# Optimization experiments

Measured on AMD Instinct MI355X. Metric: run time of the kernel, lower is better.

## Reference

```python
import jax, jax.numpy as jnp
import numpy as np

IN_CH = 64
OUT_CH = 64
MODES = 16
BATCH, H, W = 16, 128, 128


def setup_inputs() -> dict:
    key = jax.random.key(0)
    k1, k2, k3 = jax.random.split(key, 3)
    scale = 1.0 / (IN_CH * OUT_CH)
    x = jax.random.normal(k1, (BATCH, H, W, IN_CH), dtype=jnp.float32)
    weights_real = (scale * jax.random.normal(k2, (IN_CH, OUT_CH, MODES, MODES))).astype(jnp.float32)
    weights_imag = (scale * jax.random.normal(k3, (IN_CH, OUT_CH, MODES, MODES))).astype(jnp.float32)
    return {"x": x, "weights_real": weights_real, "weights_imag": weights_imag}


def reference(x, weights_real, weights_imag):
    # x: (b, h, w, c_in)
    b, h, w, _ = x.shape
    modes = weights_real.shape[-1]
    out_ch = weights_real.shape[1]

    xc = jnp.transpose(x, (0, 3, 1, 2))               # (b, c_in, h, w)
    x_ft = jnp.fft.rfft2(xc, norm="ortho")           # (b, c_in, h, w//2+1) complex64

    # Complex spectral weights; the torch double loop over (i, j) is exactly
    # a per-mode channel contraction over the low-frequency block.
    Wc = (weights_real + 1j * weights_imag).astype(jnp.complex64)
    out_modes = jnp.einsum("bixy,ioxy->boxy", x_ft[:, :, :modes, :modes], Wc)

    out_ft = jnp.zeros((b, out_ch, h, w // 2 + 1), dtype=jnp.complex64)
    out_ft = out_ft.at[:, :, :modes, :modes].set(out_modes)

    y = jnp.fft.irfft2(out_ft, s=(h, w), norm="ortho")  # (b, c_out, h, w)
    return jnp.transpose(y, (0, 2, 3, 1))                # (b, h, w, c_out)
```

## Files before the change

### kernel.cpp

```cpp
#include <hip/hip_runtime.h>

#define NB 16
#define NH 128
#define NW 128
#define NC 64
#define NO 64
#define NM 16

#define OFF_WTR  0
#define OFF_WTI  (OFF_WTR + 1048576)
#define OFF_AR   (OFF_WTI + 1048576)
#define OFF_AI   (OFF_AR + 2097152)
#define OFF_XR   (OFF_AI + 2097152)
#define OFF_XI   (OFF_XR + 262144)
#define OFF_OR   (OFF_XI + 262144)
#define OFF_OI   (OFF_OR + 262144)

#define R2F 0.70710678118654752f

constexpr float CQ[33] = {
  1.000000000f, 0.998795456f, 0.995184727f, 0.989176510f,
  0.980785280f, 0.970031253f, 0.956940336f, 0.941544065f,
  0.923879533f, 0.903989293f, 0.881921264f, 0.857728610f,
  0.831469612f, 0.803207531f, 0.773010453f, 0.740951125f,
  0.707106781f, 0.671558955f, 0.634393284f, 0.595699304f,
  0.555570233f, 0.514102744f, 0.471396737f, 0.427555093f,
  0.382683432f, 0.336889853f, 0.290284677f, 0.242980180f,
  0.195090322f, 0.146730474f, 0.098017140f, 0.049067674f,
  0.000000000f };

__host__ __device__ constexpr float twcos(int t) {
  t &= 127;
  return (t <= 32) ? CQ[t] : (t < 64) ? -CQ[64 - t] : (t <= 96) ? -CQ[t - 64] : CQ[128 - t];
}
__host__ __device__ constexpr float twsin(int t) { return twcos(t + 96); }

template<int T>
__device__ __forceinline__ void caccN_t(float gr, float gi, float& ar, float& ai) {
  constexpr int t = T & 127;
  if constexpr (t == 0)       { ar += gr; ai += gi; }
  else if constexpr (t == 64) { ar -= gr; ai -= gi; }
  else if constexpr (t == 32) { ar += gi; ai -= gr; }
  else if constexpr (t == 96) { ar -= gi; ai += gr; }
  else {
    constexpr float c = twcos(t), s = twsin(t);
    ar = fmaf(gr, c, fmaf(gi, s, ar));
    ai = fmaf(gi, c, fmaf(-gr, s, ai));
  }
}
template<int T>
__device__ __forceinline__ void caccP_t(float gr, float gi, float& ar, float& ai) {
  constexpr int t = T & 127;
  if constexpr (t == 0)       { ar += gr; ai += gi; }
  else if constexpr (t == 64) { ar -= gr; ai -= gi; }
  else if constexpr (t == 32) { ar -= gi; ai += gr; }
  else if constexpr (t == 96) { ar += gi; ai -= gr; }
  else {
    constexpr float c = twcos(t), s = twsin(t);
    ar = fmaf(gr, c, fmaf(-gi, s, ar));
    ai = fmaf(gi, c, fmaf(gr, s, ai));
  }
}
template<int T>
__device__ __forceinline__ void crotN_t(float& ar, float& ai) {
  constexpr int t = T & 127;
  if constexpr (t == 0) {}
  else if constexpr (t == 64) { ar = -ar; ai = -ai; }
  else if constexpr (t == 32) { const float r = ar; ar = ai; ai = -r; }
  else if constexpr (t == 96) { const float r = ar; ar = -ai; ai = r; }
  else {
    constexpr float c = twcos(t), s = twsin(t);
    const float r = ar;
    ar = fmaf(r, c, ai * s);
    ai = fmaf(ai, c, -r * s);
  }
}
template<int T>
__device__ __forceinline__ void crotP_t(float& ar, float& ai) {
  constexpr int t = T & 127;
  if constexpr (t == 0) {}
  else if constexpr (t == 64) { ar = -ar; ai = -ai; }
  else if constexpr (t == 32) { const float r = ar; ar = -ai; ai = r; }
  else if constexpr (t == 96) { const float r = ar; ar = ai;  ai = -r; }
  else {
    constexpr float c = twcos(t), s = twsin(t);
    const float r = ar;
    ar = fmaf(r, c, -(ai * s));
    ai = fmaf(ai, c, r * s);
  }
}

__global__ __launch_bounds__(256) void k_wt(const float* __restrict__ wre,
                                            const float* __restrict__ wim,
                                            float* __restrict__ wtr,
                                            float* __restrict__ wti) {
  __shared__ float buf[64 * 257];
  const int i = blockIdx.x & 63;
  const float* src = (blockIdx.x < 64) ? wre : wim;
  float* dst       = (blockIdx.x < 64) ? wtr : wti;
  const float* s = src + (size_t)i * 16384;
  for (int t = threadIdx.x; t < 16384; t += 256) {
    int o = t >> 8, kk = t & 255;
    buf[o * 257 + kk] = s[t];
  }
  __syncthreads();
  for (int t = threadIdx.x; t < 16384; t += 256) {
    int kk = t >> 6, o = t & 63;
    dst[(size_t)kk * 4096 + i * 64 + o] = buf[o * 257 + kk];
  }
}

template<int K>
__device__ __forceinline__ void k1_init(float (&Tr)[16], float (&Ti)[16],
                                        float (&Rr)[16], float (&Ri)[16]) {
  if constexpr (K < 16) {
    Tr[K] = 0.f; Ti[K] = 0.f; Rr[K] = 1.f; Ri[K] = 0.f;
    k1_init<K + 1>(Tr, Ti, Rr, Ri);
  }
}
template<int W1>
__device__ __forceinline__ void k1_ld8(const float* xp, int w0, float (&v)[8]) {
  if constexpr (W1 < 8) {
    v[W1] = xp[(W1 * 16 + w0) * NC];
    k1_ld8<W1 + 1>(xp, w0, v);
  }
}
template<int W1>
__device__ __forceinline__ void k1_cp8(float (&a)[8], const float (&b)[8]) {
  if constexpr (W1 < 8) { a[W1] = b[W1]; k1_cp8<W1 + 1>(a, b); }
}
template<int KY>
__device__ __forceinline__ void k1_acc(float g0r, float g4r, float g1r, float g1i,
                                       float g2r, float g2i, float g3r, float g3i,
                                       float (&Tr)[16], float (&Ti)[16],
                                       float (&Rr)[16], float (&Ri)[16]) {
  if constexpr (KY < 16) {
    constexpr int p = KY & 7;
    if constexpr (p == 0 || p == 4) {
      const float gr = (p == 0) ? g0r : g4r;
      Tr[KY] = fmaf(gr, Rr[KY], Tr[KY]);
      Ti[KY] = fmaf(gr, Ri[KY], Ti[KY]);
    } else {
      float gr, gi;
      if constexpr (p == 1)      { gr = g1r; gi = g1i; }
      else if constexpr (p == 2) { gr = g2r; gi = g2i; }
      else if constexpr (p == 3) { gr = g3r; gi = g3i; }
      else if constexpr (p == 5) { gr = g3r; gi = -g3i; }
      else if constexpr (p == 6) { gr = g2r; gi = -g2i; }
      else                       { gr = g1r; gi = -g1i; }
      Tr[KY] = fmaf(gr, Rr[KY], fmaf(-gi, Ri[KY], Tr[KY]));
      Ti[KY] = fmaf(gr, Ri[KY], fmaf( gi, Rr[KY], Ti[KY]));
    }
    crotN_t<KY>(Rr[KY], Ri[KY]);
    k1_acc<KY + 1>(g0r, g4r, g1r, g1i, g2r, g2i, g3r, g3i, Tr, Ti, Rr, Ri);
  }
}
template<int KY>
__device__ __forceinline__ void k1_store(float* t1r, float* t1i,
                                         const float (&Tr)[16], const float (&Ti)[16]) {
  if constexpr (KY < 16) {
    t1r[(size_t)KY * (NH * NC)] = Tr[KY];
    t1i[(size_t)KY * (NH * NC)] = Ti[KY];
    k1_store<KY + 1>(t1r, t1i, Tr, Ti);
  }
}

__global__ __launch_bounds__(256, 2) void k1_wdft(const float* __restrict__ x,
                                                  float* __restrict__ t1r,
                                                  float* __restrict__ t1i) {
  const int wid  = threadIdx.x >> 6;
  const int lane = threadIdx.x & 63;
  const int slab = blockIdx.x * 4 + wid;
  const float* xp = x + (size_t)slab * (NW * NC) + lane;
  float Tr[16], Ti[16], Rr[16], Ri[16];
  k1_init<0>(Tr, Ti, Rr, Ri);
  float xv[8], nx[8];
  k1_ld8<0>(xp, 0, xv);
  for (int w0 = 0; w0 < 16; ++w0) {
    if (w0 < 15) k1_ld8<0>(xp, w0 + 1, nx);
    const float s0 = xv[0] + xv[4], d0 = xv[0] - xv[4];
    const float s1 = xv[1] + xv[5], d1 = xv[1] - xv[5];
    const float s2 = xv[2] + xv[6], d2 = xv[2] - xv[6];
    const float s3 = xv[3] + xv[7], d3 = xv[3] - xv[7];
    const float e0 = s0 + s2, e1 = s0 - s2;
    const float f0 = s1 + s3, f1 = s1 - s3;
    const float u = R2F * (d1 - d3), v = R2F * (d1 + d3);
    const float g0r = e0 + f0;
    const float g4r = e0 - f0;
    const float g1r = d0 + u, g1i = -(d2 + v);
    const float g2r = e1,     g2i = -f1;
    const float g3r = d0 - u, g3i = d2 - v;
    k1_acc<0>(g0r, g4r, g1r, g1i, g2r, g2i, g3r, g3i, Tr, Ti, Rr, Ri);
    k1_cp8<0>(xv, nx);
  }
  const int b = slab >> 7, h = slab & 127;
  const size_t base = ((size_t)b * 2048 + h) * NC + lane;
  k1_store<0>(t1r + base, t1i + base, Tr, Ti);
}

template<int K>
__device__ __forceinline__ void k2a_zero(float (&Ar)[16], float (&Ai)[16]) {
  if constexpr (K < 16) { Ar[K] = 0.f; Ai[K] = 0.f; k2a_zero<K + 1>(Ar, Ai); }
}
template<int KX, int J>
__device__ __forceinline__ void k2a_kx(float re, float im, float (&Ar)[16], float (&Ai)[16]) {
  if constexpr (KX < 16) {
    caccN_t<(KX * J) & 127>(re, im, Ar[KX], Ai[KX]);
    k2a_kx<KX + 1, J>(re, im, Ar, Ai);
  }
}
template<int J>
__device__ __forceinline__ void k2a_j(const float* pr, const float* pi,
                                      float (&Ar)[16], float (&Ai)[16]) {
  if constexpr (J < 8) {
    const float re = pr[J * NC];
    const float im = pi[J * NC];
    k2a_kx<0, J>(re, im, Ar, Ai);
    k2a_j<J + 1>(pr, pi, Ar, Ai);
  }
}
template<int G, int KX>
__device__ __forceinline__ void k2a_rotg(float (&Ar)[16], float (&Ai)[16]) {
  if constexpr (KX < 16) {
    crotN_t<(8 * KX * G) & 127>(Ar[KX], Ai[KX]);
    k2a_rotg<G, KX + 1>(Ar, Ai);
  }
}
template<int KX>
__device__ __forceinline__ void k2a_ldsw(float* pr, float* pi,
                                         const float (&Ar)[16], const float (&Ai)[16]) {
  if constexpr (KX < 16) {
    pr[KX * 64] = Ar[KX]; pi[KX * 64] = Ai[KX];
    k2a_ldsw<KX + 1>(pr, pi, Ar, Ai);
  }
}
template<int KX>
__device__ __forceinline__ void k2a_ldsa(float* pr, float* pi,
                                         const float (&Ar)[16], const float (&Ai)[16]) {
  if constexpr (KX < 16) {
    pr[KX * 64] += Ar[KX]; pi[KX * 64] += Ai[KX];
    k2a_ldsa<KX + 1>(pr, pi, Ar, Ai);
  }
}

__global__ __launch_bounds__(1024, 4) void k2a_hdft(const float* __restrict__ t1r,
                                                    const float* __restrict__ t1i,
                                                    float* __restrict__ xre,
                                                    float* __restrict__ xim) {
  __shared__ float lpr[8][16][64];
  __shared__ float lpi[8][16][64];
  const int bk   = blockIdx.x;
  const int q    = threadIdx.x >> 6;
  const int lane = threadIdx.x & 63;
  const float* pr = t1r + (size_t)bk * (NH * NC) + (q * 8) * NC + lane;
  const float* pi = t1i + (size_t)bk * (NH * NC) + (q * 8) * NC + lane;
  float Ar[16], Ai[16];
  k2a_zero<0>(Ar, Ai);
  k2a_j<0>(pr, pi, Ar, Ai);
  switch (q) {
    case 1:  k2a_rotg<1, 0>(Ar, Ai);  break;
    case 2:  k2a_rotg<2, 0>(Ar, Ai);  break;
    case 3:  k2a_rotg<3, 0>(Ar, Ai);  break;
    case 4:  k2a_rotg<4, 0>(Ar, Ai);  break;
    case 5:  k2a_rotg<5, 0>(Ar, Ai);  break;
    case 6:  k2a_rotg<6, 0>(Ar, Ai);  break;
    case 7:  k2a_rotg<7, 0>(Ar, Ai);  break;
    case 8:  k2a_rotg<8, 0>(Ar, Ai);  break;
    case 9:  k2a_rotg<9, 0>(Ar, Ai);  break;
    case 10: k2a_rotg<10, 0>(Ar, Ai); break;
    case 11: k2a_rotg<11, 0>(Ar, Ai); break;
    case 12: k2a_rotg<12, 0>(Ar, Ai); break;
    case 13: k2a_rotg<13, 0>(Ar, Ai); break;
    case 14: k2a_rotg<14, 0>(Ar, Ai); break;
    case 15: k2a_rotg<15, 0>(Ar, Ai); break;
    default: break;
  }
  float* wpr = &lpr[q & 7][0][lane];
  float* wpi = &lpi[q & 7][0][lane];
  if (q < 8) k2a_ldsw<0>(wpr, wpi, Ar, Ai);
  __syncthreads();
  if (q >= 8) k2a_ldsa<0>(wpr, wpi, Ar, Ai);
  __syncthreads();
  const int kx = threadIdx.x >> 6;
  const int i  = threadIdx.x & 63;
  float sr = 0.f, si = 0.f;
#pragma unroll
  for (int p = 0; p < 8; ++p) { sr += lpr[p][kx][i]; si += lpi[p][kx][i]; }
  const int b = bk >> 4, ky = bk & 15;
  const size_t idx = (size_t)(kx * NM + ky) * (NB * NC) + b * NC + i;
  xre[idx] = sr;
  xim[idx] = si;
}

__global__ __launch_bounds__(256, 2) void k2b_mix(const float* __restrict__ xre,
                                                  const float* __restrict__ xim,
                                                  const float* __restrict__ wtr,
                                                  const float* __restrict__ wti,
                                                  float* __restrict__ ore,
                                                  float* __restrict__ oim) {
  __shared__ __align__(16) float lwr[4096], lwi[4096];
  __shared__ __align__(16) float lxr[1024], lxi[1024];
  const int kk = blockIdx.x;
  for (int t = threadIdx.x; t < 4096; t += 256) {
    lwr[t] = wtr[(size_t)kk * 4096 + t];
    lwi[t] = wti[(size_t)kk * 4096 + t];
  }
  for (int t = threadIdx.x; t < 1024; t += 256) {
    lxr[t] = xre[(size_t)kk * 1024 + t];
    lxi[t] = xim[(size_t)kk * 1024 + t];
  }
  __syncthreads();
  const int o  = threadIdx.x & 63;
  const int bq = threadIdx.x >> 6;
  float accr[4] = {0, 0, 0, 0}, acci[4] = {0, 0, 0, 0};
  for (int iq = 0; iq < 16; ++iq) {
    float xrv[4][4], xiv[4][4];
#pragma unroll
    for (int p = 0; p < 4; ++p) {
      const int b = bq * 4 + p;
      float4 vr = ((const float4*)lxr)[b * 16 + iq];
      float4 vi = ((const float4*)lxi)[b * 16 + iq];
      xrv[p][0] = vr.x; xrv[p][1] = vr.y; xrv[p][2] = vr.z; xrv[p][3] = vr.w;
      xiv[p][0] = vi.x; xiv[p][1] = vi.y; xiv[p][2] = vi.z; xiv[p][3] = vi.w;
    }
#pragma unroll
    for (int j = 0; j < 4; ++j) {
      const int i2 = iq * 4 + j;
      const float wr = lwr[i2 * 64 + o];
      const float wi = lwi[i2 * 64 + o];
#pragma unroll
      for (int p = 0; p < 4; ++p) {
        accr[p] = fmaf(xrv[p][j], wr, fmaf(-xiv[p][j], wi, accr[p]));
        acci[p] = fmaf(xrv[p][j], wi, fmaf(xiv[p][j], wr, acci[p]));
      }
    }
  }
#pragma unroll
  for (int p = 0; p < 4; ++p) {
    const int b = bq * 4 + p;
    ore[(size_t)kk * 1024 + b * 64 + o] = accr[p];
    oim[(size_t)kk * 1024 + b * 64 + o] = acci[p];
  }
}

__global__ __launch_bounds__(256, 2) void k3_hidft(const float* __restrict__ ore,
                                                   const float* __restrict__ oim,
                                                   float* __restrict__ t2r,
                                                   float* __restrict__ t2i) {
  const int b = blockIdx.x >> 5, hq = blockIdx.x & 31;
  const int q = threadIdx.x >> 6, lane = threadIdx.x & 63;
  const int ky0 = q * 4;
  float sc[4], ss[4];
  {
    const int h0 = 4 * hq;
    float wr = 1.f, wi = 0.f;
    if (h0 & 4)  crotP_t<4>(wr, wi);
    if (h0 & 8)  crotP_t<8>(wr, wi);
    if (h0 & 16) crotP_t<16>(wr, wi);
    if (h0 & 32) crotP_t<32>(wr, wi);
    if (h0 & 64) crotP_t<64>(wr, wi);
    sc[0] = wr; ss[0] = wi;
    crotP_t<1>(wr, wi); sc[1] = wr; ss[1] = wi;
    crotP_t<1>(wr, wi); sc[2] = wr; ss[2] = wi;
    crotP_t<1>(wr, wi); sc[3] = wr; ss[3] = wi;
  }
  float Rr[4] = {1.f, 1.f, 1.f, 1.f}, Ri[4] = {0.f, 0.f, 0.f, 0.f};
  float tr[4][4], ti[4][4];
#pragma unroll
  for (int j = 0; j < 4; ++j)
#pragma unroll
    for (int k = 0; k < 4; ++k) { tr[j][k] = 0.f; ti[j][k] = 0.f; }
  const size_t obase = (size_t)b * NO + lane;
  for (int kx = 0; kx < 16; ++kx) {
    float orv[4], oiv[4];
#pragma unroll
    for (int k = 0; k < 4; ++k) {
      const size_t idx = (size_t)(kx * 16 + ky0 + k) * (NB * NO) + obase;
      orv[k] = ore[idx];
      oiv[k] = oim[idx];
    }
#pragma unroll
    for (int j = 0; j < 4; ++j)
#pragma unroll
      for (int k = 0; k < 4; ++k) {
        tr[j][k] = fmaf(orv[k], Rr[j], fmaf(-oiv[k], Ri[j], tr[j][k]));
        ti[j][k] = fmaf(orv[k], Ri[j], fmaf( oiv[k], Rr[j], ti[j][k]));
      }
#pragma unroll
    for (int j = 0; j < 4; ++j) {
      const float nr = fmaf(Rr[j], sc[j], -(Ri[j] * ss[j]));
      const float ni = fmaf(Rr[j], ss[j], Ri[j] * sc[j]);
      Rr[j] = nr; Ri[j] = ni;
    }
  }
#pragma unroll
  for (int j = 0; j < 4; ++j) {
    const int h = hq * 4 + j;
#pragma unroll
    for (int k = 0; k < 4; ++k) {
      const int ky = ky0 + k;
      const float scale = (ky == 0 ? 1.0f : 2.0f) * (1.0f / 16384.0f);
      const size_t idx = ((size_t)(b * NH + h) * NM + ky) * NO + lane;
      t2r[idx] = tr[j][k] * scale;
      t2i[idx] = ti[j][k] * scale;
    }
  }
}

template<int KY>
__device__ __forceinline__ void k5_load(const float* pr, const float* pi,
                                        float (&Tr)[16], float (&Ti)[16]) {
  if constexpr (KY < 16) {
    Tr[KY] = pr[KY * NO];
    Ti[KY] = pi[KY * NO];
    k5_load<KY + 1>(pr, pi, Tr, Ti);
  }
}
template<int KY, int W0>
__device__ __forceinline__ void k5_u(const float (&Tr)[16], const float (&Ti)[16],
                                     float (&Ur)[8], float (&Ui)[8]) {
  if constexpr (KY < 16) {
    caccP_t<(KY * W0) & 127>(Tr[KY], Ti[KY], Ur[KY & 7], Ui[KY & 7]);
    k5_u<KY + 1, W0>(Tr, Ti, Ur, Ui);
  }
}
template<int P>
__device__ __forceinline__ void k5_uzero(float (&Ur)[8], float (&Ui)[8]) {
  if constexpr (P < 8) { Ur[P] = 0.f; Ui[P] = 0.f; k5_uzero<P + 1>(Ur, Ui); }
}
template<int W0>
__device__ __forceinline__ void k5_w0(const float (&Tr)[16], const float (&Ti)[16],
                                      float* yp) {
  if constexpr (W0 < 16) {
    float Ur[8], Ui[8];
    k5_uzero<0>(Ur, Ui);
    k5_u<0, W0>(Tr, Ti, Ur, Ui);
    const float A  = Ur[0], B = Ur[4];
    const float Cr = Ur[2] + Ur[6], Ci = Ui[2] - Ui[6];
    const float Dr = Ur[1] + Ur[7], Di = Ui[1] - Ui[7];
    const float Er = Ur[3] + Ur[5], Ei = Ui[3] - Ui[5];
    const float P = A + B, M = A - B;
    const float DE = Dr + Er, IE = Di - Ei;
    const float X1 = R2F * ((Dr - Di) - (Er + Ei));
    const float X3 = R2F * ((Dr + Di) - (Er - Ei));
    const float MmC = M - Ci, MpC = M + Ci, PpC = P + Cr, PmC = P - Cr;
    yp[(0 * 16 + W0) * NO] = PpC + DE;
    yp[(4 * 16 + W0) * NO] = PpC - DE;
    yp[(2 * 16 + W0) * NO] = PmC - IE;
    yp[(6 * 16 + W0) * NO] = PmC + IE;
    yp[(1 * 16 + W0) * NO] = MmC + X1;
    yp[(5 * 16 + W0) * NO] = MmC - X1;
    yp[(3 * 16 + W0) * NO] = MpC - X3;
    yp[(7 * 16 + W0) * NO] = MpC + X3;
    k5_w0<W0 + 1>(Tr, Ti, yp);
  }
}

__global__ __launch_bounds__(256, 2) void k5_widft(const float* __restrict__ t2r,
                                                   const float* __restrict__ t2i,
                                                   float* __restrict__ y) {
  const int wid  = threadIdx.x >> 6;
  const int lane = threadIdx.x & 63;
  const int slab = blockIdx.x * 4 + wid;
  const float* pr = t2r + (size_t)slab * (NM * NO) + lane;
  const float* pi = t2i + (size_t)slab * (NM * NO) + lane;
  float Tr[16], Ti[16];
  k5_load<0>(pr, pi, Tr, Ti);
  float* yp = y + (size_t)slab * (NW * NO) + lane;
  k5_w0<0>(Tr, Ti, yp);
}

extern "C" void kernel_launch(void* const* d_in, const int* in_sizes, int n_in,
                              void* d_out, int out_size, void* d_ws, size_t ws_size,
                              hipStream_t stream) {
  const float* x   = (const float*)d_in[0];
  const float* wre = (const float*)d_in[1];
  const float* wim = (const float*)d_in[2];
  float* ws  = (float*)d_ws;
  float* wtr = ws + OFF_WTR;
  float* wti = ws + OFF_WTI;
  float* ar  = ws + OFF_AR;
  float* ai  = ws + OFF_AI;
  float* xr  = ws + OFF_XR;
  float* xi  = ws + OFF_XI;
  float* orr = ws + OFF_OR;
  float* oii = ws + OFF_OI;
  float* y   = (float*)d_out;

  k_wt<<<128, 256, 0, stream>>>(wre, wim, wtr, wti);
  k1_wdft<<<512, 256, 0, stream>>>(x, ar, ai);
  k2a_hdft<<<NB * NM, 1024, 0, stream>>>(ar, ai, xr, xi);
  k2b_mix<<<NM * NM, 256, 0, stream>>>(xr, xi, wtr, wti, orr, oii);
  k3_hidft<<<512, 256, 0, stream>>>(orr, oii, ar, ai);
  k5_widft<<<512, 256, 0, stream>>>(ar, ai, y);
}
```

Before: 168.9 us.

## Split W-DFT and W-IDFT slabs across two waves, widen mixing kernel

The forward W-direction DFT kernel now splits each slab's 16 w0 iterations between two waves. Each wave starts its twiddle rotation at the matching phase, and the partial sums are combined through shared memory before the store. The inverse W kernel likewise splits its 16 output columns between two waves, and the mode-mixing kernel uses 512 threads with 2 batches per thread instead of 4. The aim is to double the number of waves and raise occupancy in these latency-bound stages. The cost is a shared-memory reduction and barrier in k1, and duplicated loads of the T coefficients in k5.

```diff
diff --git a/kernel.cpp b/kernel.cpp
--- a/kernel.cpp
+++ b/kernel.cpp
@@ -111,11 +111,16 @@
 }
 
 template<int K>
-__device__ __forceinline__ void k1_init(float (&Tr)[16], float (&Ti)[16],
-                                        float (&Rr)[16], float (&Ri)[16]) {
+__device__ __forceinline__ void k1_zeroT(float (&Tr)[16], float (&Ti)[16]) {
+  if constexpr (K < 16) { Tr[K] = 0.f; Ti[K] = 0.f; k1_zeroT<K + 1>(Tr, Ti); }
+}
+template<int K, int P0>
+__device__ __forceinline__ void k1_initR(float (&Rr)[16], float (&Ri)[16]) {
   if constexpr (K < 16) {
-    Tr[K] = 0.f; Ti[K] = 0.f; Rr[K] = 1.f; Ri[K] = 0.f;
-    k1_init<K + 1>(Tr, Ti, Rr, Ri);
+    constexpr int t = (K * P0) & 127;
+    Rr[K] = twcos(t);
+    Ri[K] = -twsin(t);
+    k1_initR<K + 1, P0>(Rr, Ri);
   }
 }
 template<int W1>
@@ -155,6 +160,22 @@
     k1_acc<KY + 1>(g0r, g4r, g1r, g1i, g2r, g2i, g3r, g3i, Tr, Ti, Rr, Ri);
   }
 }
+template<int K>
+__device__ __forceinline__ void k1_ldswr(float* p, const float (&Tr)[16], const float (&Ti)[16]) {
+  if constexpr (K < 16) {
+    p[K * 64]        = Tr[K];
+    p[(16 + K) * 64] = Ti[K];
+    k1_ldswr<K + 1>(p, Tr, Ti);
+  }
+}
+template<int K>
+__device__ __forceinline__ void k1_ldsadd(const float* p, float (&Tr)[16], float (&Ti)[16]) {
+  if constexpr (K < 16) {
+    Tr[K] += p[K * 64];
+    Ti[K] += p[(16 + K) * 64];
+    k1_ldsadd<K + 1>(p, Tr, Ti);
+  }
+}
 template<int KY>
 __device__ __forceinline__ void k1_store(float* t1r, float* t1i,
                                          const float (&Tr)[16], const float (&Ti)[16]) {
@@ -165,19 +186,25 @@
   }
 }
 
-__global__ __launch_bounds__(256, 2) void k1_wdft(const float* __restrict__ x,
+__global__ __launch_bounds__(256, 4) void k1_wdft(const float* __restrict__ x,
                                                   float* __restrict__ t1r,
                                                   float* __restrict__ t1i) {
-  const int wid  = threadIdx.x >> 6;
+  __shared__ float lds[2][32][64];
+  const int wv   = threadIdx.x >> 6;
   const int lane = threadIdx.x & 63;
-  const int slab = blockIdx.x * 4 + wid;
+  const int sq   = wv >> 1;
+  const int half = wv & 1;
+  const int slab = blockIdx.x * 2 + sq;
   const float* xp = x + (size_t)slab * (NW * NC) + lane;
   float Tr[16], Ti[16], Rr[16], Ri[16];
-  k1_init<0>(Tr, Ti, Rr, Ri);
+  k1_zeroT<0>(Tr, Ti);
+  if (half == 0) k1_initR<0, 0>(Rr, Ri);
+  else           k1_initR<0, 8>(Rr, Ri);
   float xv[8], nx[8];
-  k1_ld8<0>(xp, 0, xv);
-  for (int w0 = 0; w0 < 16; ++w0) {
-    if (w0 < 15) k1_ld8<0>(xp, w0 + 1, nx);
+  k1_ld8<0>(xp, half * 8, xv);
+  for (int it = 0; it < 8; ++it) {
+    const int w0 = half * 8 + it;
+    if (it < 7) k1_ld8<0>(xp, w0 + 1, nx);
     const float s0 = xv[0] + xv[4], d0 = xv[0] - xv[4];
     const float s1 = xv[1] + xv[5], d1 = xv[1] - xv[5];
     const float s2 = xv[2] + xv[6], d2 = xv[2] - xv[6];
@@ -193,9 +220,15 @@
     k1_acc<0>(g0r, g4r, g1r, g1i, g2r, g2i, g3r, g3i, Tr, Ti, Rr, Ri);
     k1_cp8<0>(xv, nx);
   }
-  const int b = slab >> 7, h = slab & 127;
-  const size_t base = ((size_t)b * 2048 + h) * NC + lane;
-  k1_store<0>(t1r + base, t1i + base, Tr, Ti);
+  float* lp = &lds[sq][0][lane];
+  if (half) k1_ldswr<0>(lp, Tr, Ti);
+  __syncthreads();
+  if (!half) {
+    k1_ldsadd<0>(lp, Tr, Ti);
+    const int b = slab >> 7, h = slab & 127;
+    const size_t base = ((size_t)b * 2048 + h) * NC + lane;
+    k1_store<0>(t1r + base, t1i + base, Tr, Ti);
+  }
 }
 
 template<int K>
@@ -292,7 +325,7 @@
   xim[idx] = si;
 }
 
-__global__ __launch_bounds__(256, 2) void k2b_mix(const float* __restrict__ xre,
+__global__ __launch_bounds__(512, 2) void k2b_mix(const float* __restrict__ xre,
                                                   const float* __restrict__ xim,
                                                   const float* __restrict__ wtr,
                                                   const float* __restrict__ wti,
@@ -301,23 +334,23 @@
   __shared__ __align__(16) float lwr[4096], lwi[4096];
   __shared__ __align__(16) float lxr[1024], lxi[1024];
   const int kk = blockIdx.x;
-  for (int t = threadIdx.x; t < 4096; t += 256) {
+  for (int t = threadIdx.x; t < 4096; t += 512) {
     lwr[t] = wtr[(size_t)kk * 4096 + t];
     lwi[t] = wti[(size_t)kk * 4096 + t];
   }
-  for (int t = threadIdx.x; t < 1024; t += 256) {
+  for (int t = threadIdx.x; t < 1024; t += 512) {
     lxr[t] = xre[(size_t)kk * 1024 + t];
     lxi[t] = xim[(size_t)kk * 1024 + t];
   }
   __syncthreads();
   const int o  = threadIdx.x & 63;
   const int bq = threadIdx.x >> 6;
-  float accr[4] = {0, 0, 0, 0}, acci[4] = {0, 0, 0, 0};
+  float accr[2] = {0, 0}, acci[2] = {0, 0};
   for (int iq = 0; iq < 16; ++iq) {
-    float xrv[4][4], xiv[4][4];
-#pragma unroll
-    for (int p = 0; p < 4; ++p) {
-      const int b = bq * 4 + p;
+    float xrv[2][4], xiv[2][4];
+#pragma unroll
+    for (int p = 0; p < 2; ++p) {
+      const int b = bq * 2 + p;
       float4 vr = ((const float4*)lxr)[b * 16 + iq];
       float4 vi = ((const float4*)lxi)[b * 16 + iq];
       xrv[p][0] = vr.x; xrv[p][1] = vr.y; xrv[p][2] = vr.z; xrv[p][3] = vr.w;
@@ -329,15 +362,15 @@
       const float wr = lwr[i2 * 64 + o];
       const float wi = lwi[i2 * 64 + o];
 #pragma unroll
-      for (int p = 0; p < 4; ++p) {
+      for (int p = 0; p < 2; ++p) {
         accr[p] = fmaf(xrv[p][j], wr, fmaf(-xiv[p][j], wi, accr[p]));
         acci[p] = fmaf(xrv[p][j], wi, fmaf(xiv[p][j], wr, acci[p]));
       }
     }
   }
 #pragma unroll
-  for (int p = 0; p < 4; ++p) {
-    const int b = bq * 4 + p;
+  for (int p = 0; p < 2; ++p) {
+    const int b = bq * 2 + p;
     ore[(size_t)kk * 1024 + b * 64 + o] = accr[p];
     oim[(size_t)kk * 1024 + b * 64 + o] = acci[p];
   }
@@ -428,10 +461,10 @@
 __device__ __forceinline__ void k5_uzero(float (&Ur)[8], float (&Ui)[8]) {
   if constexpr (P < 8) { Ur[P] = 0.f; Ui[P] = 0.f; k5_uzero<P + 1>(Ur, Ui); }
 }
-template<int W0>
+template<int W0, int W0END>
 __device__ __forceinline__ void k5_w0(const float (&Tr)[16], const float (&Ti)[16],
                                       float* yp) {
-  if constexpr (W0 < 16) {
+  if constexpr (W0 < W0END) {
     float Ur[8], Ui[8];
     k5_uzero<0>(Ur, Ui);
     k5_u<0, W0>(Tr, Ti, Ur, Ui);
@@ -452,22 +485,25 @@
     yp[(5 * 16 + W0) * NO] = MmC - X1;
     yp[(3 * 16 + W0) * NO] = MpC - X3;
     yp[(7 * 16 + W0) * NO] = MpC + X3;
-    k5_w0<W0 + 1>(Tr, Ti, yp);
-  }
-}
-
-__global__ __launch_bounds__(256, 2) void k5_widft(const float* __restrict__ t2r,
+    k5_w0<W0 + 1, W0END>(Tr, Ti, yp);
+  }
+}
+
+__global__ __launch_bounds__(256, 4) void k5_widft(const float* __restrict__ t2r,
                                                    const float* __restrict__ t2i,
                                                    float* __restrict__ y) {
-  const int wid  = threadIdx.x >> 6;
+  const int wv   = threadIdx.x >> 6;
   const int lane = threadIdx.x & 63;
-  const int slab = blockIdx.x * 4 + wid;
+  const int sq   = wv >> 1;
+  const int half = wv & 1;
+  const int slab = blockIdx.x * 2 + sq;
   const float* pr = t2r + (size_t)slab * (NM * NO) + lane;
   const float* pi = t2i + (size_t)slab * (NM * NO) + lane;
   float Tr[16], Ti[16];
   k5_load<0>(pr, pi, Tr, Ti);
   float* yp = y + (size_t)slab * (NW * NO) + lane;
-  k5_w0<0>(Tr, Ti, yp);
+  if (half == 0) k5_w0<0, 8>(Tr, Ti, yp);
+  else           k5_w0<8, 16>(Tr, Ti, yp);
 }
 
 extern "C" void kernel_launch(void* const* d_in, const int* in_sizes, int n_in,
@@ -488,9 +524,9 @@
   float* y   = (float*)d_out;
 
   k_wt<<<128, 256, 0, stream>>>(wre, wim, wtr, wti);
-  k1_wdft<<<512, 256, 0, stream>>>(x, ar, ai);
+  k1_wdft<<<1024, 256, 0, stream>>>(x, ar, ai);
   k2a_hdft<<<NB * NM, 1024, 0, stream>>>(ar, ai, xr, xi);
-  k2b_mix<<<NM * NM, 256, 0, stream>>>(xr, xi, wtr, wti, orr, oii);
+  k2b_mix<<<NM * NM, 512, 0, stream>>>(xr, xi, wtr, wti, orr, oii);
   k3_hidft<<<512, 256, 0, stream>>>(orr, oii, ar, ai);
-  k5_widft<<<512, 256, 0, stream>>>(ar, ai, y);
-}
+  k5_widft<<<1024, 256, 0, stream>>>(ar, ai, y);
+}
```

New measurement: 155.6 us. 1.09x faster.
